# Performance work log

Measured on AMD Instinct MI355X. Metric: run time of the kernel, lower is better.

The kernel has to match this reference:

```python
import jax, jax.numpy as jnp
import numpy as np

E = 2048      # embed_size
H = 16        # heads_size
D_HEAD = E // H          # 128
D_ROPE = 32
SPLIT = D_HEAD - D_ROPE  # 96
C = 512       # d_kv_comp
B, S = 2, 2048
ROT_SCALE = 40.0


def _rotary_emb(seq_len):
    # inv_freq has d_rope//4 entries; emb is [S, d_rope//2]
    half = D_ROPE // 2
    inv_freq = 1.0 / (10000.0 ** (jnp.arange(0, half, 2, dtype=jnp.float32) / half))
    t = jnp.arange(seq_len, dtype=jnp.float32) / ROT_SCALE
    freqs = jnp.einsum('i,j->ij', t, inv_freq)
    return jnp.concatenate([freqs, freqs], axis=-1)  # [S, d_rope//2]


def _rotate_half(x):
    x1, x2 = jnp.split(x, 2, axis=-1)
    return jnp.concatenate([-x2, x1], axis=-1)


def _apply_rotary(x, cos, sin):
    rd = cos.shape[-1]
    x_rot, x_base = x[..., :rd], x[..., rd:]
    x_rot = x_rot * cos + _rotate_half(x_rot) * sin
    return jnp.concatenate([x_rot, x_base], axis=-1)


def setup_inputs() -> dict:
    key = jax.random.key(0)
    ks = jax.random.split(key, 10)

    def xav(k, shape):
        fan_in, fan_out = shape
        lim = float(np.sqrt(6.0 / (fan_in + fan_out)))
        return jax.random.uniform(k, shape, jnp.float32, -lim, lim)

    return {
        'h': jax.random.normal(ks[0], (B, S, E), jnp.float32),
        'W_dkv': xav(ks[1], (E, C)), 'b_dkv': jnp.zeros((C,), jnp.float32),
        'W_dq':  xav(ks[2], (E, C)), 'b_dq':  jnp.zeros((C,), jnp.float32),
        'W_uk':  xav(ks[3], (C, H * SPLIT)),  'b_uk': jnp.zeros((H * SPLIT,), jnp.float32),
        'W_uv':  xav(ks[4], (C, H * D_HEAD)), 'b_uv': jnp.zeros((H * D_HEAD,), jnp.float32),
        'W_uq':  xav(ks[5], (C, H * SPLIT)),  'b_uq': jnp.zeros((H * SPLIT,), jnp.float32),
        'W_qr':  xav(ks[6], (C, H * D_ROPE)), 'b_qr': jnp.zeros((H * D_ROPE,), jnp.float32),
        'W_kr':  xav(ks[7], (E, H * D_ROPE)), 'b_kr': jnp.zeros((H * D_ROPE,), jnp.float32),
        'W_out': xav(ks[8], (H * D_HEAD, E)), 'b_out': jnp.zeros((E,), jnp.float32),
    }


def reference(h, W_dkv, b_dkv, W_dq, b_dq, W_uk, b_uk, W_uv, b_uv,
              W_uq, b_uq, W_qr, b_qr, W_kr, b_kr, W_out, b_out):
    Bq, Sq, _ = h.shape
    c_kv = h @ W_dkv + b_dkv                                   # [B,S,C]
    k = (c_kv @ W_uk + b_uk).reshape(Bq, Sq, H, SPLIT)
    v = (c_kv @ W_uv + b_uv).reshape(Bq, Sq, H, D_HEAD)
    c_q = h @ W_dq + b_dq
    q_base = (c_q @ W_uq + b_uq).reshape(Bq, Sq, H, SPLIT)
    q_rot = (c_q @ W_qr + b_qr).reshape(Bq, Sq, H, D_ROPE)

    emb = _rotary_emb(Sq)                                      # [S, d_rope//2]
    cos = jnp.cos(emb)[None, :, None, :]
    sin = jnp.sin(emb)[None, :, None, :]
    q_rot = _apply_rotary(q_rot, cos, sin)
    k_rot = _apply_rotary((h @ W_kr + b_kr).reshape(Bq, Sq, H, D_ROPE), cos, sin)

    q = jnp.concatenate([q_base, q_rot], axis=-1)              # [B,S,H,d_head]
    k_full = jnp.concatenate([k, k_rot], axis=-1)

    scores = jnp.einsum('bqhd,bkhd->bhqk', q, k_full) / jnp.sqrt(jnp.float32(D_HEAD))
    causal = jnp.tril(jnp.ones((Sq, Sq), dtype=bool))
    scores = jnp.where(causal[None, None], scores, -jnp.inf)
    attn = jax.nn.softmax(scores, axis=-1)
    out = jnp.einsum('bhqk,bkhd->bqhd', attn, v).reshape(Bq, Sq, H * D_HEAD)
    out = out @ W_out + b_out
    return out, c_kv, k_rot
```

## Files before the change

### kernel.cpp

```cpp
#include <hip/hip_runtime.h>
#include <hip/hip_bf16.h>

#define B_   2
#define S_   2048
#define E_   2048
#define H_   16
#define DH_  128
#define DR_  32
#define SP_  96
#define C_   512
#define M_   (B_ * S_)

#define LOG2E 1.4426950408889634f

typedef __attribute__((ext_vector_type(8))) short short8;
typedef __attribute__((ext_vector_type(4))) float floatx4;

__device__ __forceinline__ float bfu(unsigned short u) {
  return __uint_as_float((unsigned)u << 16);
}
__device__ __forceinline__ unsigned short f2bf(float f) {
  unsigned u = __float_as_uint(f);
  return (unsigned short)((u + 0x7fff + ((u >> 16) & 1)) >> 16);
}

__device__ __forceinline__ void gload16(const void* g, void* l) {
  __builtin_amdgcn_global_load_lds(
      (const __attribute__((address_space(1))) void*)g,
      (__attribute__((address_space(3))) void*)l, 16, 0, 0);
}

__global__ __launch_bounds__(256) void f2bf_kernel(
    const float* __restrict__ src, unsigned short* __restrict__ dst) {
  size_t i = ((size_t)blockIdx.x * 256 + threadIdx.x) * 4;
  float4 v = *(const float4*)(src + i);
  ushort4 w;
  w.x = f2bf(v.x); w.y = f2bf(v.y); w.z = f2bf(v.z); w.w = f2bf(v.w);
  *(ushort4*)(dst + i) = w;
}

struct TEnt { const float* W; unsigned short* Wt; int K, N, ntiles, nx; };
struct TTab { TEnt e[8]; };

__global__ __launch_bounds__(256) void transpose_all_kernel(TTab tab) {
  __shared__ unsigned short T[32][33];
  int rem = blockIdx.x;
  const float* W = nullptr; unsigned short* Wt = nullptr;
  int K = 0, N = 0, nx = 1;
  bool done = false;
#pragma unroll
  for (int j = 0; j < 8; j++) {
    if (!done) {
      if (rem < tab.e[j].ntiles) {
        W = tab.e[j].W; Wt = tab.e[j].Wt;
        K = tab.e[j].K; N = tab.e[j].N; nx = tab.e[j].nx;
        done = true;
      } else {
        rem -= tab.e[j].ntiles;
      }
    }
  }
  int n0 = (rem % nx) * 32, k0 = (rem / nx) * 32;
  int t = threadIdx.x, lane = t & 31, grp = t >> 5;
#pragma unroll
  for (int p = 0; p < 4; p++) {
    int k = p * 8 + grp;
    T[lane][k] = f2bf(W[(size_t)(k0 + k) * N + n0 + lane]);
  }
  __syncthreads();
#pragma unroll
  for (int p = 0; p < 4; p++) {
    int n = p * 8 + grp;
    Wt[(size_t)(n0 + n) * K + k0 + lane] = T[n][lane];
  }
}

struct Seg {
  float* outF;
  unsigned short* outB;
  const float* bias;
  const float* biasM;
  int orow, chunk, gstride, obase, nstart, ileave;
  float oscale;
};

__global__ __launch_bounds__(256) void mfma_gemm(
    const unsigned short* __restrict__ A, const unsigned short* __restrict__ Wt,
    Seg s0, Seg s1, Seg s2, int K) {
  __shared__ unsigned short As0[128 * 32];
  __shared__ unsigned short Bs0[128 * 32];
  __shared__ unsigned short As1[128 * 32];
  __shared__ unsigned short Bs1[128 * 32];
  int tid = threadIdx.x;
  int lane = tid & 63, wave = tid >> 6;
  int l16 = lane & 15, quad = lane >> 4;

  int gx = gridDim.x;
  int nwg = gx * gridDim.y;
  int flat = blockIdx.y * gx + blockIdx.x;
  int w = (flat & 7) * (nwg >> 3) + (flat >> 3);
  int by = w / gx, bx = w - by * gx;
  int bm = by * 128, bn = bx * 128;
  int wm = (wave & 1) * 64, wn = (wave >> 1) * 64;

  floatx4 acc[4][4];
#pragma unroll
  for (int mt = 0; mt < 4; mt++)
#pragma unroll
    for (int nt = 0; nt < 4; nt++) acc[mt][nt] = (floatx4){0.f, 0.f, 0.f, 0.f};

  int c0 = wave * 2, c1 = c0 + 1;
  int srow = lane >> 2, scol = (lane & 3) * 8;
  const unsigned short* Ag0 = A + (size_t)(bm + c0 * 16 + srow) * K + scol;
  const unsigned short* Ag1 = A + (size_t)(bm + c1 * 16 + srow) * K + scol;
  const unsigned short* Bg0 = Wt + (size_t)(bn + c0 * 16 + srow) * K + scol;
  const unsigned short* Bg1 = Wt + (size_t)(bn + c1 * 16 + srow) * K + scol;

#define GSTAGE(kk, Asb, Bsb) do {            \
    gload16(Ag0 + (kk), &Asb[c0 * 512]);     \
    gload16(Ag1 + (kk), &Asb[c1 * 512]);     \
    gload16(Bg0 + (kk), &Bsb[c0 * 512]);     \
    gload16(Bg1 + (kk), &Bsb[c1 * 512]); } while (0)

#define GCOMPUTE(Asb, Bsb) do {                                            \
    short8 af[4], bfv[4];                                                  \
    _Pragma("unroll")                                                      \
    for (int mt = 0; mt < 4; mt++)                                         \
      af[mt] = *(const short8*)&Asb[(wm + mt * 16 + l16) * 32 + quad * 8]; \
    _Pragma("unroll")                                                      \
    for (int nt = 0; nt < 4; nt++)                                         \
      bfv[nt] = *(const short8*)&Bsb[(wn + nt * 16 + l16) * 32 + quad * 8];\
    _Pragma("unroll")                                                      \
    for (int mt = 0; mt < 4; mt++)                                         \
      _Pragma("unroll")                                                    \
      for (int nt = 0; nt < 4; nt++)                                       \
        acc[mt][nt] = __builtin_amdgcn_mfma_f32_16x16x32_bf16(             \
            af[mt], bfv[nt], acc[mt][nt], 0, 0, 0); } while (0)

  GSTAGE(0, As0, Bs0);
  __syncthreads();
  for (int k0 = 0; k0 < K; k0 += 64) {
    GSTAGE(k0 + 32, As1, Bs1);
    GCOMPUTE(As0, Bs0);
    __syncthreads();
    if (k0 + 64 < K) GSTAGE(k0 + 64, As0, Bs0);
    GCOMPUTE(As1, Bs1);
    __syncthreads();
  }
#undef GSTAGE
#undef GCOMPUTE

  Seg sg = (bn >= s2.nstart) ? s2 : ((bn >= s1.nstart) ? s1 : s0);

#pragma unroll
  for (int mt = 0; mt < 4; mt++) {
    int m0 = bm + wm + mt * 16 + quad * 4;
    float bm4[4] = {0.f, 0.f, 0.f, 0.f};
    if (sg.biasM) {
#pragma unroll
      for (int r = 0; r < 4; r++) bm4[r] = sg.biasM[m0 + r];
    }
#pragma unroll
    for (int nt = 0; nt < 4; nt++) {
      int n = bn + wn + nt * 16 + l16;
      int nl = n - sg.nstart;
      float bv = sg.biasM ? 0.f : sg.bias[nl];
      int ncol = sg.obase + (nl / sg.chunk) * sg.gstride + (nl % sg.chunk);
      if (sg.ileave)
        ncol = (ncol & ~31) | ((ncol & 15) << 1) | ((ncol >> 4) & 1);
#pragma unroll
      for (int r = 0; r < 4; r++) {
        float val = (acc[mt][nt][r] + (sg.biasM ? bm4[r] : bv)) * sg.oscale;
        size_t idx = (size_t)(m0 + r) * sg.orow + ncol;
        if (sg.outF) sg.outF[idx] = val;
        if (sg.outB) sg.outB[idx] = f2bf(val);
      }
    }
  }
}

__global__ __launch_bounds__(256) void rope_kernel(
    unsigned short* __restrict__ qf, unsigned short* __restrict__ kf,
    float* __restrict__ krot_out) {
  int idx = blockIdx.x * 256 + threadIdx.x;
  int j  = idx & 7;
  int h  = (idx >> 3) & (H_ - 1);
  int bs = idx >> 7;
  if (bs >= M_) return;
  int s = bs & (S_ - 1);
  float t = (float)s / 40.0f;
  float ang = t * exp2f(-1.6609640474436813f * (float)j);
  float c = cosf(ang), sn = sinf(ang);

  size_t base = (size_t)bs * 2048 + h * 128 + 96;
  float x0 = bfu(qf[base + j]), x1 = bfu(qf[base + j + 8]);
  qf[base + j]     = f2bf(x0 * c - x1 * sn);
  qf[base + j + 8] = f2bf(x1 * c + x0 * sn);

  float y0 = bfu(kf[base + j]), y1 = bfu(kf[base + j + 8]);
  float r0 = y0 * c - y1 * sn;
  float r1 = y1 * c + y0 * sn;
  kf[base + j]     = f2bf(r0);
  kf[base + j + 8] = f2bf(r1);

  size_t ko = (size_t)bs * (H_ * DR_) + h * DR_;
  krot_out[ko + j]      = r0;
  krot_out[ko + j + 8]  = r1;
  krot_out[ko + 16 + j] = bfu(kf[base + 16 + j]);
  krot_out[ko + 24 + j] = bfu(kf[base + 24 + j]);
}

#define KST 136
#define VST 40
#define PST 40
__global__ __launch_bounds__(256) void attn_kernel(
    const unsigned short* __restrict__ qf, const unsigned short* __restrict__ kf,
    const unsigned short* __restrict__ vt, unsigned short* __restrict__ ao) {
  __shared__ unsigned short Ks[2][32 * KST];
  __shared__ unsigned short Vs[2][128 * VST];
  __shared__ unsigned short Ps[4][16 * PST];

  int bid0 = blockIdx.x;
  int xcd  = bid0 & 7;
  int idx  = bid0 >> 3;
  int bh   = xcd * 4 + (idx >> 4);
  int jp   = idx & 15;
  int h    = bh & 15;
  int b    = bh >> 4;

  int tid  = threadIdx.x;
  int wave = tid >> 6;
  int lane = tid & 63;
  int l16  = lane & 15;
  int quad = lane >> 4;

  int srow  = tid >> 3;
  int sd0   = (tid & 7) * 16;
  int vrow  = tid >> 1;
  int vhalf = (tid & 1) * 16;

  const unsigned short* kbase =
      kf + ((size_t)(b * S_ + srow)) * 2048 + h * 128 + sd0;
  const unsigned short* vbase =
      vt + ((size_t)(h * 128 + vrow)) * 4096 + b * 2048 + vhalf;

#define ACOMPUTE() do {                                                       \
    int kt0 = t << 5;                                                         \
    if (kt0 <= qg_hi) {                                                       \
      const unsigned short* Kc = Ks[cur];                                     \
      const unsigned short* Vc = Vs[cur];                                     \
      floatx4 s0v = {0.f,0.f,0.f,0.f}, s1v = {0.f,0.f,0.f,0.f};               \
      __builtin_amdgcn_s_setprio(1);                                          \
      _Pragma("unroll")                                                       \
      for (int c = 0; c < 4; c++) {                                           \
        short8 kfr = *(const short8*)&Kc[l16 * KST + c * 32 + quad * 8];      \
        s0v = __builtin_amdgcn_mfma_f32_16x16x32_bf16(qfrag[c], kfr, s0v, 0, 0, 0); \
      }                                                                       \
      _Pragma("unroll")                                                       \
      for (int c = 0; c < 4; c++) {                                           \
        short8 kfr = *(const short8*)&Kc[(16 + l16) * KST + c * 32 + quad * 8]; \
        s1v = __builtin_amdgcn_mfma_f32_16x16x32_bf16(qfrag[c], kfr, s1v, 0, 0, 0); \
      }                                                                       \
      __builtin_amdgcn_s_setprio(0);                                          \
      unsigned short* P = Ps[wave];                                           \
      bool diag = (kt0 + 31 > qg_lo);                                         \
      _Pragma("unroll")                                                       \
      for (int r = 0; r < 4; r++) {                                           \
        float p0 = exp2f(fminf(s0v[r], 80.f));                                \
        float p1 = exp2f(fminf(s1v[r], 80.f));                                \
        if (diag) {                                                           \
          int q_r = qg_lo + quad * 4 + r;                                     \
          if (kt0 + l16 > q_r)      p0 = 0.f;                                 \
          if (kt0 + 16 + l16 > q_r) p1 = 0.f;                                 \
        }                                                                     \
        unsigned pk;                                                          \
        asm("v_cvt_pk_bf16_f32 %0, %1, %2" : "=v"(pk) : "v"(p0), "v"(p1));    \
        *(unsigned*)&P[(quad * 4 + r) * PST + 2 * l16] = pk;                  \
        lpart[r] += p0 + p1;                                                  \
      }                                                                       \
      short8 pfrag = *(const short8*)&P[l16 * PST + quad * 8];                \
      __builtin_amdgcn_s_setprio(1);                                          \
      _Pragma("unroll")                                                       \
      for (int dt = 0; dt < 8; dt++) {                                        \
        short8 vfr = *(const short8*)&Vc[(dt * 16 + l16) * VST + quad * 8];   \
        Oacc[dt] = __builtin_amdgcn_mfma_f32_16x16x32_bf16(pfrag, vfr, Oacc[dt], 0, 0, 0); \
      }                                                                       \
      __builtin_amdgcn_s_setprio(0);                                          \
    } } while (0)

#define ABODY(W0, W1, W2, W3, L0, L1, L2, L3) do {                            \
    unsigned short* kdw = &Ks[cur ^ 1][srow * KST + sd0];                     \
    unsigned short* vdw = &Vs[cur ^ 1][vrow * VST + vhalf];                   \
    *(short8*)kdw = W0; *(short8*)(kdw + 8) = W1;                             \
    *(short8*)vdw = W2; *(short8*)(vdw + 8) = W3;                             \
    { int tf = (t + 2 < nkt) ? t + 2 : nkt - 1;                               \
      const unsigned short* ksrc = kbase + (size_t)tf * 65536;                \
      const unsigned short* vsrc = vbase + tf * 32;                           \
      L0 = *(const short8*)ksrc; L1 = *(const short8*)(ksrc + 8);             \
      L2 = *(const short8*)vsrc; L3 = *(const short8*)(vsrc + 8); }           \
    ACOMPUTE();                                                               \
    __syncthreads();                                                          \
    cur ^= 1; } while (0)

  for (int half = 0; half < 2; half++) {
    int jj = half ? (31 - jp) : jp;
    int q0 = jj << 6;

    int qrow = q0 + wave * 16 + l16;
    const unsigned short* qbase =
        qf + ((size_t)(b * S_ + qrow)) * 2048 + h * 128 + quad * 8;
    short8 qfrag[4];
#pragma unroll
    for (int c = 0; c < 4; c++) qfrag[c] = *(const short8*)(qbase + c * 32);

    floatx4 Oacc[8];
#pragma unroll
    for (int dt = 0; dt < 8; dt++) Oacc[dt] = (floatx4){0.f, 0.f, 0.f, 0.f};
    float lpart[4] = {0.f, 0.f, 0.f, 0.f};

    int qg_lo = q0 + wave * 16;
    int qg_hi = qg_lo + 15;
    int nkt = 2 * jj + 2;

    short8 rA0, rA1, rA2, rA3, rB0, rB1, rB2, rB3;
    rA0 = *(const short8*)kbase;       rA1 = *(const short8*)(kbase + 8);
    rA2 = *(const short8*)vbase;       rA3 = *(const short8*)(vbase + 8);
    {
      unsigned short* kdw = &Ks[0][srow * KST + sd0];
      unsigned short* vdw = &Vs[0][vrow * VST + vhalf];
      *(short8*)kdw = rA0; *(short8*)(kdw + 8) = rA1;
      *(short8*)vdw = rA2; *(short8*)(vdw + 8) = rA3;
    }
    {
      const unsigned short* ksrc = kbase + 65536;
      const unsigned short* vsrc = vbase + 32;
      rA0 = *(const short8*)ksrc; rA1 = *(const short8*)(ksrc + 8);
      rA2 = *(const short8*)vsrc; rA3 = *(const short8*)(vsrc + 8);
    }
    __syncthreads();

    int cur = 0, t = 0;
    while (true) {
      ABODY(rA0, rA1, rA2, rA3, rB0, rB1, rB2, rB3);
      if (++t >= nkt) break;
      ABODY(rB0, rB1, rB2, rB3, rA0, rA1, rA2, rA3);
      if (++t >= nkt) break;
    }

    float linv[4];
#pragma unroll
    for (int r = 0; r < 4; r++) {
      float ls = lpart[r];
#pragma unroll
      for (int sh = 1; sh < 16; sh <<= 1) ls += __shfl_xor(ls, sh);
      linv[r] = 1.0f / ls;
    }
    int qg = q0 + wave * 16 + quad * 4;
#pragma unroll
    for (int r = 0; r < 4; r++) {
      unsigned short* dst = ao + ((size_t)(b * S_ + qg + r)) * 2048 + h * 128 + l16;
#pragma unroll
      for (int dt = 0; dt < 8; dt++) dst[dt * 16] = f2bf(Oacc[dt][r] * linv[r]);
    }
  }
#undef ABODY
#undef ACOMPUTE
}

static inline Seg mkseg(float* oF, unsigned short* oB, const float* bias,
                        const float* biasM, int orow, int chunk, int gstride,
                        int obase, int nstart, int ileave, float oscale) {
  Seg s;
  s.outF = oF; s.outB = oB; s.bias = bias; s.biasM = biasM;
  s.orow = orow; s.chunk = chunk; s.gstride = gstride;
  s.obase = obase; s.nstart = nstart; s.ileave = ileave; s.oscale = oscale;
  return s;
}
static inline Seg segnone() {
  return mkseg(nullptr, nullptr, nullptr, nullptr, 1, 1, 1, 0, 0x7fffffff, 0, 1.f);
}
static inline TEnt mktent(const float* W, unsigned short* Wt, int K, int N,
                          int ntiles, int nx) {
  TEnt e;
  e.W = W; e.Wt = Wt; e.K = K; e.N = N; e.ntiles = ntiles; e.nx = nx;
  return e;
}

extern "C" void kernel_launch(void* const* d_in, const int* in_sizes, int n_in,
                              void* d_out, int out_size, void* d_ws, size_t ws_size,
                              hipStream_t stream) {
  const float* h     = (const float*)d_in[0];
  const float* W_dkv = (const float*)d_in[1];
  const float* b_dkv = (const float*)d_in[2];
  const float* W_dq  = (const float*)d_in[3];
  const float* b_dq  = (const float*)d_in[4];
  const float* W_uk  = (const float*)d_in[5];
  const float* b_uk  = (const float*)d_in[6];
  const float* W_uv  = (const float*)d_in[7];
  const float* b_uv  = (const float*)d_in[8];
  const float* W_uq  = (const float*)d_in[9];
  const float* b_uq  = (const float*)d_in[10];
  const float* W_qr  = (const float*)d_in[11];
  const float* b_qr  = (const float*)d_in[12];
  const float* W_kr  = (const float*)d_in[13];
  const float* b_kr  = (const float*)d_in[14];
  const float* W_out = (const float*)d_in[15];
  const float* b_out = (const float*)d_in[16];

  float* out      = (float*)d_out;
  float* out_ckv  = out + (size_t)M_ * E_;
  float* out_krot = out_ckv + (size_t)M_ * C_;

  unsigned short* w16 = (unsigned short*)d_ws;
  unsigned short* h_bf   = w16;
  unsigned short* q_bf   = w16 + 8388608;
  unsigned short* k_bf   = w16 + 16777216;
  unsigned short* vt_bf  = w16 + 25165824;
  unsigned short* ao_bf  = w16 + 33554432;
  unsigned short* ckv_bf = w16 + 41943040;
  unsigned short* cq_bf  = w16 + 44040192;
  unsigned short* Wt_dkv = w16 + 46137344;
  unsigned short* Wt_dq  = w16 + 47185920;
  unsigned short* Wt_kr  = w16 + 48234496;
  unsigned short* Wt_uk  = w16 + 49283072;
  unsigned short* Wt_uv  = w16 + 50069504;
  unsigned short* Wt_uq  = w16 + 51118080;
  unsigned short* Wt_qr  = w16 + 51904512;
  unsigned short* Wt_out = w16 + 52166656;

  dim3 blk(256);
  const float qscale = 0.08838834764831845f * LOG2E;

  f2bf_kernel<<<8192, blk, 0, stream>>>(h, h_bf);

  TTab tab;
  tab.e[0] = mktent(W_dkv, Wt_dkv, E_, C_,       1024, 16);
  tab.e[1] = mktent(W_dq,  Wt_dq,  E_, C_,       1024, 16);
  tab.e[2] = mktent(W_kr,  Wt_kr,  E_, H_ * DR_, 1024, 16);
  tab.e[3] = mktent(W_uk,  Wt_uk,  C_, H_ * SP_,  768, 48);
  tab.e[4] = mktent(W_uv,  Wt_uv,  C_, H_ * DH_, 1024, 64);
  tab.e[5] = mktent(W_uq,  Wt_uq,  C_, H_ * SP_,  768, 48);
  tab.e[6] = mktent(W_qr,  Wt_qr,  C_, H_ * DR_,  256, 16);
  tab.e[7] = mktent(W_out, Wt_out, E_, E_,       4096, 64);
  transpose_all_kernel<<<9984, blk, 0, stream>>>(tab);

  mfma_gemm<<<dim3(1536 / 128, M_ / 128), blk, 0, stream>>>(
      h_bf, Wt_dkv,
      mkseg(out_ckv, ckv_bf, b_dkv, nullptr, C_, C_, C_, 0, 0, 0, 1.f),
      mkseg(nullptr, cq_bf,  b_dq,  nullptr, C_, C_, C_, 0, 512, 0, 1.f),
      mkseg(nullptr, k_bf,   b_kr,  nullptr, 2048, DR_, DH_, SP_, 1024, 0, 1.f),
      E_);
  mfma_gemm<<<dim3((H_ * SP_) / 128, M_ / 128), blk, 0, stream>>>(
      ckv_bf, Wt_uk,
      mkseg(nullptr, k_bf, b_uk, nullptr, 2048, SP_, DH_, 0, 0, 0, 1.f),
      segnone(), segnone(), C_);
  mfma_gemm<<<dim3(M_ / 128, (H_ * DH_) / 128), blk, 0, stream>>>(
      Wt_uv, ckv_bf,
      mkseg(nullptr, vt_bf, nullptr, b_uv, M_, M_, M_, 0, 0, 1, 1.f),
      segnone(), segnone(), C_);
  mfma_gemm<<<dim3(2048 / 128, M_ / 128), blk, 0, stream>>>(
      cq_bf, Wt_uq,
      mkseg(nullptr, q_bf, b_uq, nullptr, 2048, SP_, DH_, 0, 0, 0, qscale),
      mkseg(nullptr, q_bf, b_qr, nullptr, 2048, DR_, DH_, SP_, 1536, 0, qscale),
      segnone(), C_);

  rope_kernel<<<(M_ * H_ * 8) / 256, blk, 0, stream>>>(q_bf, k_bf, out_krot);
  attn_kernel<<<B_ * H_ * 16, blk, 0, stream>>>(q_bf, k_bf, vt_bf, ao_bf);

  mfma_gemm<<<dim3(E_ / 128, M_ / 128), blk, 0, stream>>>(
      ao_bf, Wt_out,
      mkseg(out, nullptr, b_out, nullptr, E_, E_, E_, 0, 0, 0, 1.f),
      segnone(), segnone(), E_);
}
```

Measured before the change: 375.8 us.

## Share K/V tiles across paired query blocks with 64-key chunks and XOR-swizzled LDS

The attention kernel now processes its two query blocks (high and low) together in a single pass over key chunks, so each K/V tile loaded into shared memory serves both blocks instead of being reloaded per block. Key chunks grow from 32 to 64 rows, and the K/V LDS tiles switch from padded strides to an XOR-swizzled layout to avoid bank conflicts. The cost is doubled accumulator registers (two O tiles and two Q fragment sets) and a larger LDS footprint, with launch bounds requesting 2 blocks per CU.

```diff
diff --git a/kernel.cpp b/kernel.cpp
--- a/kernel.cpp
+++ b/kernel.cpp
@@ -210,14 +210,12 @@
   krot_out[ko + 24 + j] = bfu(kf[base + 24 + j]);
 }
 
-#define KST 136
-#define VST 40
-#define PST 40
-__global__ __launch_bounds__(256) void attn_kernel(
+#define PST 72
+__global__ __launch_bounds__(256, 2) void attn_kernel(
     const unsigned short* __restrict__ qf, const unsigned short* __restrict__ kf,
     const unsigned short* __restrict__ vt, unsigned short* __restrict__ ao) {
-  __shared__ unsigned short Ks[2][32 * KST];
-  __shared__ unsigned short Vs[2][128 * VST];
+  __shared__ unsigned short Ks[2][64 * 128];
+  __shared__ unsigned short Vs[2][128 * 64];
   __shared__ unsigned short Ps[4][16 * PST];
 
   int bid0 = blockIdx.x;
@@ -227,144 +225,174 @@
   int jp   = idx & 15;
   int h    = bh & 15;
   int b    = bh >> 4;
+  int jjh  = 31 - jp;
+  int jjl  = jp;
+  int q0h  = jjh << 6, q0l = jjl << 6;
+  int nchunks = jjh + 1;
 
   int tid  = threadIdx.x;
   int wave = tid >> 6;
   int lane = tid & 63;
   int l16  = lane & 15;
   int quad = lane >> 4;
-
-  int srow  = tid >> 3;
-  int sd0   = (tid & 7) * 16;
-  int vrow  = tid >> 1;
-  int vhalf = (tid & 1) * 16;
-
-  const unsigned short* kbase =
-      kf + ((size_t)(b * S_ + srow)) * 2048 + h * 128 + sd0;
-  const unsigned short* vbase =
-      vt + ((size_t)(h * 128 + vrow)) * 4096 + b * 2048 + vhalf;
-
-#define ACOMPUTE() do {                                                       \
-    int kt0 = t << 5;                                                         \
-    if (kt0 <= qg_hi) {                                                       \
-      const unsigned short* Kc = Ks[cur];                                     \
-      const unsigned short* Vc = Vs[cur];                                     \
-      floatx4 s0v = {0.f,0.f,0.f,0.f}, s1v = {0.f,0.f,0.f,0.f};               \
-      __builtin_amdgcn_s_setprio(1);                                          \
+  int x7   = l16 & 7;
+
+  int krow = tid >> 2;
+  int kst  = (tid & 3) * 4;
+  int vrow = tid >> 1;
+  int vst  = (tid & 1) * 4;
+  const unsigned short* kg =
+      kf + ((size_t)(b * S_ + krow)) * 2048 + h * 128 + kst * 8;
+  const unsigned short* vg =
+      vt + ((size_t)(h * 128 + vrow)) * 4096 + b * 2048 + vst * 8;
+  int kwl[4], vwl[4];
+#pragma unroll
+  for (int i = 0; i < 4; i++) {
+    kwl[i] = krow * 128 + (((kst + i) ^ (krow & 7)) * 8);
+    vwl[i] = vrow * 64  + (((vst + i) ^ (vrow & 7)) * 8);
+  }
+
+  short8 qfh[4], qfl[4];
+  {
+    const unsigned short* qb =
+        qf + ((size_t)(b * S_ + q0h + wave * 16 + l16)) * 2048 + h * 128 + quad * 8;
+#pragma unroll
+    for (int c = 0; c < 4; c++) qfh[c] = *(const short8*)(qb + c * 32);
+  }
+  {
+    const unsigned short* qb =
+        qf + ((size_t)(b * S_ + q0l + wave * 16 + l16)) * 2048 + h * 128 + quad * 8;
+#pragma unroll
+    for (int c = 0; c < 4; c++) qfl[c] = *(const short8*)(qb + c * 32);
+  }
+
+  floatx4 OaccH[8], OaccL[8];
+#pragma unroll
+  for (int dt = 0; dt < 8; dt++) {
+    OaccH[dt] = (floatx4){0.f, 0.f, 0.f, 0.f};
+    OaccL[dt] = (floatx4){0.f, 0.f, 0.f, 0.f};
+  }
+  float lpH[4] = {0.f, 0.f, 0.f, 0.f};
+  float lpL[4] = {0.f, 0.f, 0.f, 0.f};
+  int qgh = q0h + wave * 16;
+  int qgl = q0l + wave * 16;
+
+#define SCOMPUTE(QF, OC, LP, QG, DIAG) do {                                   \
+    const unsigned short* Kc = Ks[cur];                                       \
+    const unsigned short* Vc = Vs[cur];                                       \
+    floatx4 sv[4];                                                            \
+    _Pragma("unroll")                                                         \
+    for (int nt = 0; nt < 4; nt++) sv[nt] = (floatx4){0.f, 0.f, 0.f, 0.f};    \
+    __builtin_amdgcn_s_setprio(1);                                            \
+    _Pragma("unroll")                                                         \
+    for (int nt = 0; nt < 4; nt++)                                            \
       _Pragma("unroll")                                                       \
       for (int c = 0; c < 4; c++) {                                           \
-        short8 kfr = *(const short8*)&Kc[l16 * KST + c * 32 + quad * 8];      \
-        s0v = __builtin_amdgcn_mfma_f32_16x16x32_bf16(qfrag[c], kfr, s0v, 0, 0, 0); \
+        short8 kfr = *(const short8*)&Kc[(nt * 16 + l16) * 128 +              \
+                                         ((4 * c + quad) ^ x7) * 8];          \
+        sv[nt] = __builtin_amdgcn_mfma_f32_16x16x32_bf16(QF[c], kfr, sv[nt],  \
+                                                         0, 0, 0);            \
       }                                                                       \
-      _Pragma("unroll")                                                       \
-      for (int c = 0; c < 4; c++) {                                           \
-        short8 kfr = *(const short8*)&Kc[(16 + l16) * KST + c * 32 + quad * 8]; \
-        s1v = __builtin_amdgcn_mfma_f32_16x16x32_bf16(qfrag[c], kfr, s1v, 0, 0, 0); \
-      }                                                                       \
-      __builtin_amdgcn_s_setprio(0);                                          \
-      unsigned short* P = Ps[wave];                                           \
-      bool diag = (kt0 + 31 > qg_lo);                                         \
+    __builtin_amdgcn_s_setprio(0);                                            \
+    unsigned short* P = Ps[wave];                                             \
+    _Pragma("unroll")                                                         \
+    for (int ks = 0; ks < 2; ks++)                                            \
       _Pragma("unroll")                                                       \
       for (int r = 0; r < 4; r++) {                                           \
-        float p0 = exp2f(fminf(s0v[r], 80.f));                                \
-        float p1 = exp2f(fminf(s1v[r], 80.f));                                \
-        if (diag) {                                                           \
-          int q_r = qg_lo + quad * 4 + r;                                     \
-          if (kt0 + l16 > q_r)      p0 = 0.f;                                 \
-          if (kt0 + 16 + l16 > q_r) p1 = 0.f;                                 \
+        float p0 = exp2f(fminf(sv[2 * ks][r], 80.f));                         \
+        float p1 = exp2f(fminf(sv[2 * ks + 1][r], 80.f));                     \
+        if (DIAG) {                                                           \
+          int q_r = QG + quad * 4 + r;                                        \
+          int kc0 = kt0 + ks * 32 + l16;                                      \
+          if (kc0 > q_r)      p0 = 0.f;                                       \
+          if (kc0 + 16 > q_r) p1 = 0.f;                                       \
         }                                                                     \
         unsigned pk;                                                          \
         asm("v_cvt_pk_bf16_f32 %0, %1, %2" : "=v"(pk) : "v"(p0), "v"(p1));    \
-        *(unsigned*)&P[(quad * 4 + r) * PST + 2 * l16] = pk;                  \
-        lpart[r] += p0 + p1;                                                  \
+        *(unsigned*)&P[(quad * 4 + r) * PST + ks * 32 + 2 * l16] = pk;        \
+        LP[r] += p0 + p1;                                                     \
       }                                                                       \
-      short8 pfrag = *(const short8*)&P[l16 * PST + quad * 8];                \
-      __builtin_amdgcn_s_setprio(1);                                          \
-      _Pragma("unroll")                                                       \
-      for (int dt = 0; dt < 8; dt++) {                                        \
-        short8 vfr = *(const short8*)&Vc[(dt * 16 + l16) * VST + quad * 8];   \
-        Oacc[dt] = __builtin_amdgcn_mfma_f32_16x16x32_bf16(pfrag, vfr, Oacc[dt], 0, 0, 0); \
-      }                                                                       \
-      __builtin_amdgcn_s_setprio(0);                                          \
-    } } while (0)
-
-#define ABODY(W0, W1, W2, W3, L0, L1, L2, L3) do {                            \
-    unsigned short* kdw = &Ks[cur ^ 1][srow * KST + sd0];                     \
-    unsigned short* vdw = &Vs[cur ^ 1][vrow * VST + vhalf];                   \
-    *(short8*)kdw = W0; *(short8*)(kdw + 8) = W1;                             \
-    *(short8*)vdw = W2; *(short8*)(vdw + 8) = W3;                             \
-    { int tf = (t + 2 < nkt) ? t + 2 : nkt - 1;                               \
-      const unsigned short* ksrc = kbase + (size_t)tf * 65536;                \
-      const unsigned short* vsrc = vbase + tf * 32;                           \
-      L0 = *(const short8*)ksrc; L1 = *(const short8*)(ksrc + 8);             \
-      L2 = *(const short8*)vsrc; L3 = *(const short8*)(vsrc + 8); }           \
-    ACOMPUTE();                                                               \
-    __syncthreads();                                                          \
-    cur ^= 1; } while (0)
-
-  for (int half = 0; half < 2; half++) {
-    int jj = half ? (31 - jp) : jp;
-    int q0 = jj << 6;
-
-    int qrow = q0 + wave * 16 + l16;
-    const unsigned short* qbase =
-        qf + ((size_t)(b * S_ + qrow)) * 2048 + h * 128 + quad * 8;
-    short8 qfrag[4];
-#pragma unroll
-    for (int c = 0; c < 4; c++) qfrag[c] = *(const short8*)(qbase + c * 32);
-
-    floatx4 Oacc[8];
-#pragma unroll
-    for (int dt = 0; dt < 8; dt++) Oacc[dt] = (floatx4){0.f, 0.f, 0.f, 0.f};
-    float lpart[4] = {0.f, 0.f, 0.f, 0.f};
-
-    int qg_lo = q0 + wave * 16;
-    int qg_hi = qg_lo + 15;
-    int nkt = 2 * jj + 2;
-
-    short8 rA0, rA1, rA2, rA3, rB0, rB1, rB2, rB3;
-    rA0 = *(const short8*)kbase;       rA1 = *(const short8*)(kbase + 8);
-    rA2 = *(const short8*)vbase;       rA3 = *(const short8*)(vbase + 8);
+    short8 pf0 = *(const short8*)&P[l16 * PST + quad * 8];                    \
+    short8 pf1 = *(const short8*)&P[l16 * PST + 32 + quad * 8];               \
+    __builtin_amdgcn_s_setprio(1);                                            \
+    _Pragma("unroll")                                                         \
+    for (int dt = 0; dt < 8; dt++) {                                          \
+      short8 vf0 = *(const short8*)&Vc[(dt * 16 + l16) * 64 +                 \
+                                       ((quad) ^ x7) * 8];                    \
+      OC[dt] = __builtin_amdgcn_mfma_f32_16x16x32_bf16(pf0, vf0, OC[dt],      \
+                                                       0, 0, 0);              \
+      short8 vf1 = *(const short8*)&Vc[(dt * 16 + l16) * 64 +                 \
+                                       ((4 + quad) ^ x7) * 8];                \
+      OC[dt] = __builtin_amdgcn_mfma_f32_16x16x32_bf16(pf1, vf1, OC[dt],      \
+                                                       0, 0, 0);              \
+    }                                                                         \
+    __builtin_amdgcn_s_setprio(0);                                            \
+  } while (0)
+
+  short8 kr[4], vr[4];
+#pragma unroll
+  for (int i = 0; i < 4; i++) {
+    kr[i] = *(const short8*)(kg + i * 8);
+    vr[i] = *(const short8*)(vg + i * 8);
+  }
+#pragma unroll
+  for (int i = 0; i < 4; i++) {
+    *(short8*)&Ks[0][kwl[i]] = kr[i];
+    *(short8*)&Vs[0][vwl[i]] = vr[i];
+  }
+#pragma unroll
+  for (int i = 0; i < 4; i++) {
+    kr[i] = *(const short8*)(kg + 131072 + i * 8);
+    vr[i] = *(const short8*)(vg + 64 + i * 8);
+  }
+  __syncthreads();
+
+  int cur = 0;
+  for (int t = 0; t < nchunks; t++) {
+#pragma unroll
+    for (int i = 0; i < 4; i++) {
+      *(short8*)&Ks[cur ^ 1][kwl[i]] = kr[i];
+      *(short8*)&Vs[cur ^ 1][vwl[i]] = vr[i];
+    }
     {
-      unsigned short* kdw = &Ks[0][srow * KST + sd0];
-      unsigned short* vdw = &Vs[0][vrow * VST + vhalf];
-      *(short8*)kdw = rA0; *(short8*)(kdw + 8) = rA1;
-      *(short8*)vdw = rA2; *(short8*)(vdw + 8) = rA3;
-    }
-    {
-      const unsigned short* ksrc = kbase + 65536;
-      const unsigned short* vsrc = vbase + 32;
-      rA0 = *(const short8*)ksrc; rA1 = *(const short8*)(ksrc + 8);
-      rA2 = *(const short8*)vsrc; rA3 = *(const short8*)(vsrc + 8);
-    }
+      int tf = (t + 2 < nchunks) ? t + 2 : nchunks - 1;
+      const unsigned short* ksrc = kg + (size_t)tf * 131072;
+      const unsigned short* vsrc = vg + tf * 64;
+#pragma unroll
+      for (int i = 0; i < 4; i++) {
+        kr[i] = *(const short8*)(ksrc + i * 8);
+        vr[i] = *(const short8*)(vsrc + i * 8);
+      }
+    }
+    int kt0 = t << 6;
+    SCOMPUTE(qfh, OaccH, lpH, qgh, (t == jjh));
+    if (t <= jjl) SCOMPUTE(qfl, OaccL, lpL, qgl, (t == jjl));
     __syncthreads();
-
-    int cur = 0, t = 0;
-    while (true) {
-      ABODY(rA0, rA1, rA2, rA3, rB0, rB1, rB2, rB3);
-      if (++t >= nkt) break;
-      ABODY(rB0, rB1, rB2, rB3, rA0, rA1, rA2, rA3);
-      if (++t >= nkt) break;
-    }
-
+    cur ^= 1;
+  }
+#undef SCOMPUTE
+
+#pragma unroll
+  for (int side = 0; side < 2; side++) {
+    floatx4* OC = side ? OaccL : OaccH;
+    float*   LP = side ? lpL : lpH;
+    int qg = (side ? qgl : qgh) + quad * 4;
     float linv[4];
 #pragma unroll
     for (int r = 0; r < 4; r++) {
-      float ls = lpart[r];
+      float ls = LP[r];
 #pragma unroll
       for (int sh = 1; sh < 16; sh <<= 1) ls += __shfl_xor(ls, sh);
       linv[r] = 1.0f / ls;
     }
-    int qg = q0 + wave * 16 + quad * 4;
 #pragma unroll
     for (int r = 0; r < 4; r++) {
-      unsigned short* dst = ao + ((size_t)(b * S_ + qg + r)) * 2048 + h * 128 + l16;
-#pragma unroll
-      for (int dt = 0; dt < 8; dt++) dst[dt * 16] = f2bf(Oacc[dt][r] * linv[r]);
-    }
-  }
-#undef ABODY
-#undef ACOMPUTE
+      unsigned short* dst =
+          ao + ((size_t)(b * S_ + qg + r)) * 2048 + h * 128 + l16;
+#pragma unroll
+      for (int dt = 0; dt < 8; dt++) dst[dt * 16] = f2bf(OC[dt][r] * linv[r]);
+    }
+  }
 }
 
 static inline Seg mkseg(float* oF, unsigned short* oB, const float* bias,
```

After: 368.5 us. About the same (-1.9%).
